# Kernel optimization log

Measured on AMD Instinct MI355X. Metric: run time of the kernel, lower is better.

The kernel has to match this reference:

```python
import jax, jax.numpy as jnp
import numpy as np

B, S, H = 8, 2048, 1024   # batch, seq, hidden_size
E = 4                     # num_experts (world_size=1 -> all local)
C = 1024                  # kv_cache_size (cache_decrement=0 -> uniform pyramid)
R = 4                     # LoRA rank
ALPHA = 1.0
TOP_K = 2
TEMP = 1.0
KEEP = C // 2             # pyramid compressor keeps top-half by importance


def _lora(z, A, Bm):
    # LoRALayer: (z @ A) @ B scaled by alpha/rank
    return (z @ A) @ Bm * (ALPHA / A.shape[-1])


def setup_inputs() -> dict:
    key = jax.random.key(0)
    ks = jax.random.split(key, 24)
    w = lambda k, shp: jax.random.normal(k, shp, jnp.float32) * 0.02
    return {
        'x': jax.random.normal(ks[0], (B, S, H), jnp.float32),
        'query': jax.random.normal(ks[1], (B, S, H), jnp.float32),
        'Wg': w(ks[2], (H, E)), 'bg': jnp.zeros((E,), jnp.float32),
        'Wq': w(ks[3], (H, H)), 'bq': jnp.zeros((H,), jnp.float32),
        'Wk': w(ks[4], (H, H)), 'bk': jnp.zeros((H,), jnp.float32),
        'Aq': w(ks[5], (H, R)), 'Bq': w(ks[6], (R, H)),
        'Ak': w(ks[7], (H, R)), 'Bk': w(ks[8], (R, H)),
        'We': w(ks[9], (E, H, H)), 'be': jnp.zeros((E, H), jnp.float32),
        'Ae': w(ks[10], (E, H, R)), 'Be': w(ks[11], (E, R, H)),
        'Av': w(ks[12], (E, H, R)), 'Bv': w(ks[13], (E, R, H)),
        'cache_keys': jax.random.normal(ks[14], (E, C, H), jnp.float32),
        'cache_values': jax.random.normal(ks[15], (E, C, H), jnp.float32),
        'cache_imp': jax.random.uniform(ks[16], (E, C), jnp.float32),
    }


def reference(x, query, Wg, bg, Wq, bq, Wk, bk, Aq, Bq, Ak, Bk,
              We, be, Ae, Be, Av, Bv, cache_keys, cache_values, cache_imp):
    # ---- AdaptiveRouter: softmax gate, top-2 renormalized, load-balance loss ----
    probs = jax.nn.softmax((x @ Wg + bg) / TEMP, axis=-1)             # [B,S,E]
    tw, ti = jax.lax.top_k(probs, TOP_K)                              # [B,S,K]
    twn = tw / tw.sum(-1, keepdims=True)
    onehot = jax.nn.one_hot(ti, E, dtype=x.dtype)                     # [B,S,K,E]
    routing = jnp.einsum('bsk,bske->bse', twn, onehot)                # [B,S,E]
    lb_loss = E * jnp.sum(probs.mean((0, 1)) * onehot.mean((0, 1, 2)))

    # ---- compute_token_importance (query provided): LoRA-augmented q/k attention ----
    q = query @ Wq + bq + _lora(query, Aq, Bq)
    k = x @ Wk + bk + _lora(x, Ak, Bk)
    att = jax.nn.softmax(jnp.einsum('bqh,bkh->bqk', q, k) / np.sqrt(H).astype(np.float32), axis=-1)
    importance = att.sum(axis=1)                                      # [B,S] column sums

    # ---- per-expert LoRA forward + pyramid-compressed cache read ----
    def expert_fn(We_i, be_i, Ae_i, Be_i, Av_i, Bv_i, cv_i, ci_i):
        eo = x @ We_i + be_i + _lora(x, Ae_i, Be_i)                   # [B,S,H]
        idx = jax.lax.top_k(ci_i, KEEP)[1]                            # keep top-half by importance
        vals = cv_i[idx]                                              # [KEEP,H] irregular gather
        vals = vals + _lora(vals, Av_i, Bv_i)                         # value LoRA on compressed cache
        return eo + jax.lax.stop_gradient(vals.mean(0))               # cached values are detached

    outs = jax.vmap(expert_fn)(We, be, Ae, Be, Av, Bv, cache_values, cache_imp)  # [E,B,S,H]
    expert_output = jnp.einsum('ebsh,bse->bsh', outs, routing)

    # ---- cache update at ptr=0 (detached buffer mutation -> returned new state) ----
    sg = jax.lax.stop_gradient
    new_keys = cache_keys.at[:, 0].set(jnp.broadcast_to(sg(x.mean((0, 1))), (E, H)))
    new_values = cache_values.at[:, 0].set(sg(outs.mean((1, 2))))
    new_imp = cache_imp.at[:, 0].set(sg(importance.mean()))
    return expert_output, lb_loss, new_keys, new_values, new_imp
```

## Files before the change

kernel.cpp:

```cpp
#include <hip/hip_runtime.h>

constexpr int kH    = 1024;
constexpr int kNT   = 16384;
constexpr int kE    = 4;
constexpr int kC    = 1024;
constexpr int kR    = 4;
constexpr int kKeep = 512;
constexpr float kLoraScale = 0.25f;
constexpr int kCapTiles = 136;
constexpr int kCapRows  = kCapTiles * 128;
constexpr int kNB      = kNT / 256;

constexpr size_t WS_RW     = 0;
constexpr size_t WS_G      = 65536;
constexpr size_t WS_XSUM   = 393216;
constexpr size_t WS_SHADOW = 394240;
constexpr size_t WS_TU     = 394752;
constexpr size_t WS_VBAR   = 394784;
constexpr size_t WS_FX     = 398880;
constexpr size_t WS_NEWV0  = 402976;
constexpr size_t WS_MSK    = 407072;
constexpr size_t WS_GBASE  = 411168;
constexpr size_t WS_BHIST  = 411176;
constexpr size_t WS_BOFF   = 411560;
constexpr size_t WS_RTPID  = 411944;
constexpr size_t WS_TPID   = 412088;
constexpr size_t WS_GRO    = 428472;
constexpr size_t WS_PERM   = 444856;
constexpr size_t WS_WCAT   = 462264;
constexpr size_t WS_AEXT   = 482744;
constexpr size_t WS_AEXTG  = 744888;
constexpr size_t WS_BEXT   = 1023416;
constexpr size_t WS_WET    = 1039800;
constexpr size_t WS_XG     = 3136952;

constexpr size_t OUT_LB = 16777216;
constexpr size_t OUT_NK = 16777217;

typedef __attribute__((ext_vector_type(8))) short bf16x8;
typedef __attribute__((ext_vector_type(4))) float f32x4;

__device__ __forceinline__ float wred(float v) {
#pragma unroll
  for (int off = 32; off; off >>= 1) v += __shfl_xor(v, off);
  return v;
}

__device__ __forceinline__ ushort f2bf(float f) {
  unsigned int u = __float_as_uint(f);
  u += 0x7FFFu + ((u >> 16) & 1u);
  return (ushort)(u >> 16);
}

__device__ __forceinline__ void gload16(const ushort* g, ushort* l) {
  __builtin_amdgcn_global_load_lds(
      (const __attribute__((address_space(1))) unsigned int*)g,
      (__attribute__((address_space(3))) unsigned int*)l, 16, 0, 0);
}

__device__ __forceinline__ int pid_a(int pid) { return pid < 3 ? 0 : (pid < 5 ? 1 : 2); }
__device__ __forceinline__ int pid_b(int pid) { return pid < 3 ? pid + 1 : (pid < 5 ? pid - 1 : 3); }

__global__ __launch_bounds__(256) void prep_k(
    const float* __restrict__ Wg, const float* __restrict__ Ae,
    const float* __restrict__ ci, const float* __restrict__ x,
    float* __restrict__ wcat, float* __restrict__ msk,
    float* __restrict__ xsum, int* __restrict__ perm) {
  __shared__ float imp[kC];
  const int b = blockIdx.x, tid = threadIdx.x;
  if (b < 80) {
    const int idx = b * 256 + tid;
    const int c = idx >> 10, k = idx & 1023;
    float v;
    if (c < 4) v = Wg[(size_t)k * 4 + c];
    else {
      const int e = (c - 4) >> 2, r = (c - 4) & 3;
      v = Ae[((size_t)e * kH + k) * kR + r];
    }
    wcat[(size_t)c * kH + k] = v;
  } else if (b < 96) {
    const int e = (b - 80) >> 2, part = (b - 80) & 3;
    const int c = part * 256 + tid;
    for (int i = tid; i < kC; i += 256) imp[i] = ci[(size_t)e * kC + i];
    __syncthreads();
    const float v = imp[c];
    int rank = 0;
    for (int c2 = 0; c2 < kC; ++c2) {
      const float v2 = imp[c2];
      rank += (v2 > v) || (v2 == v && c2 < c);
    }
    msk[(size_t)e * kC + c] = (rank < kKeep) ? 1.0f : 0.0f;
  } else if (b < 352) {
    const int rg = b - 96;
    const float* xp = x + (size_t)rg * 64 * kH + tid * 4;
    float s0 = 0.f, s1 = 0.f, s2 = 0.f, s3 = 0.f;
    for (int r = 0; r < 64; ++r) {
      const float4 v = *(const float4*)(xp + (size_t)r * kH);
      s0 += v.x; s1 += v.y; s2 += v.z; s3 += v.w;
    }
    atomicAdd(&xsum[tid * 4 + 0], s0);
    atomicAdd(&xsum[tid * 4 + 1], s1);
    atomicAdd(&xsum[tid * 4 + 2], s2);
    atomicAdd(&xsum[tid * 4 + 3], s3);
  } else {
    const int i = (b - 352) * 256 + tid;
    perm[i] = -1;
  }
}

__global__ __launch_bounds__(256) void router_gemm_k(
    const float* __restrict__ x, const float* __restrict__ wcat,
    float* __restrict__ G) {
  __shared__ float xs_l[128][64];
  __shared__ float wt_l[20][64];
  const int tid = threadIdx.x;
  const int t0 = blockIdx.x * 128;
  const int tok = tid & 127, half = tid >> 7, cb = half * 10;
  float acc[10] = {};
  for (int kc = 0; kc < 16; ++kc) {
#pragma unroll
    for (int i = 0; i < 8; ++i) {
      const int idx = tid + i * 256;
      const int stok = idx >> 4, sslot = idx & 15;
      const float4 v =
          *(const float4*)(x + (size_t)(t0 + stok) * kH + kc * 64 + sslot * 4);
      *(float4*)&xs_l[stok][((sslot + stok) & 15) * 4] = v;
    }
    for (int idx = tid; idx < 320; idx += 256) {
      const int c = idx >> 4, slot = idx & 15;
      *(float4*)&wt_l[c][slot * 4] =
          *(const float4*)(wcat + (size_t)c * kH + kc * 64 + slot * 4);
    }
    __syncthreads();
#pragma unroll
    for (int k4 = 0; k4 < 16; ++k4) {
      const float4 xv = *(const float4*)&xs_l[tok][((k4 + tok) & 15) * 4];
#pragma unroll
      for (int j = 0; j < 10; ++j) {
        const float4 wv = *(const float4*)&wt_l[cb + j][k4 * 4];
        acc[j] += xv.x * wv.x + xv.y * wv.y + xv.z * wv.z + xv.w * wv.w;
      }
    }
    __syncthreads();
  }
#pragma unroll
  for (int j = 0; j < 10; ++j)
    G[(size_t)(cb + j) * kNT + t0 + tok] = acc[j];
}

__global__ __launch_bounds__(256) void router_fin_k(
    const float* __restrict__ G, const float* __restrict__ bg,
    float* __restrict__ rw, float* __restrict__ shadow,
    int* __restrict__ tpid, int* __restrict__ bhist,
    ushort* __restrict__ aext) {
  __shared__ float swacc[8];
  __shared__ int ihist[6];
  const int tid = threadIdx.x;
  const int t = blockIdx.x * 256 + tid;
  const int lane = tid & 63;
  if (tid < 8) swacc[tid] = 0.f;
  if (tid < 6) ihist[tid] = 0;
  __syncthreads();
  float lg[kE];
#pragma unroll
  for (int e = 0; e < kE; ++e) lg[e] = G[(size_t)e * kNT + t] + bg[e];
  float la[kE][kR];
#pragma unroll
  for (int e = 0; e < kE; ++e)
#pragma unroll
    for (int r = 0; r < kR; ++r)
      la[e][r] = G[(size_t)(4 + e * 4 + r) * kNT + t];
  const float mx = fmaxf(fmaxf(lg[0], lg[1]), fmaxf(lg[2], lg[3]));
  float ex[kE], se = 0.f;
#pragma unroll
  for (int e = 0; e < kE; ++e) { ex[e] = __expf(lg[e] - mx); se += ex[e]; }
  float pr[kE];
#pragma unroll
  for (int e = 0; e < kE; ++e) pr[e] = ex[e] / se;
  int e1 = 0;
#pragma unroll
  for (int e = 1; e < kE; ++e) if (pr[e] > pr[e1]) e1 = e;
  int e2 = (e1 == 0) ? 1 : 0;
#pragma unroll
  for (int e = 0; e < kE; ++e) if (e != e1 && pr[e] > pr[e2]) e2 = e;
  const float s2 = pr[e1] + pr[e2];
  float rwv[kE] = {0.f, 0.f, 0.f, 0.f};
  rwv[e1] = pr[e1] / s2; rwv[e2] = pr[e2] / s2;
  *(float4*)(rw + (size_t)t * kE) = make_float4(rwv[0], rwv[1], rwv[2], rwv[3]);
  const int lo = min(e1, e2), hi = max(e1, e2);
  const int pid = (lo == 0) ? hi - 1 : ((lo == 1) ? hi + 1 : 5);
  tpid[t] = pid;
  __align__(16) ushort o[32];
#pragma unroll
  for (int e = 0; e < kE; ++e) o[e] = f2bf(rwv[e]);
#pragma unroll
  for (int e = 0; e < kE; ++e)
#pragma unroll
    for (int r = 0; r < kR; ++r)
      o[4 + e * 4 + r] = f2bf(kLoraScale * rwv[e] * la[e][r]);
#pragma unroll
  for (int i = 20; i < 32; ++i) o[i] = 0;
#pragma unroll
  for (int q = 0; q < 4; ++q)
    *(float4*)&aext[(size_t)t * 32 + q * 8] = *(float4*)&o[q * 8];
  float vals[8];
#pragma unroll
  for (int e = 0; e < kE; ++e) {
    vals[e] = pr[e];
    vals[4 + e] = ((e == e1) ? 1.f : 0.f) + ((e == e2) ? 1.f : 0.f);
  }
#pragma unroll
  for (int j = 0; j < 8; ++j) {
    vals[j] = wred(vals[j]);
    if (lane == 0) atomicAdd(&swacc[j], vals[j]);
  }
  atomicAdd(&ihist[pid], 1);
  __syncthreads();
  if (tid < 8) atomicAdd(&shadow[(blockIdx.x & 63) * 8 + tid], swacc[tid]);
  if (tid < 6) bhist[blockIdx.x * 6 + tid] = ihist[tid];
}

__global__ __launch_bounds__(256) void pscan_k(const int* __restrict__ bhist,
                                               int* __restrict__ gbase,
                                               int* __restrict__ boff,
                                               int* __restrict__ rtpid) {
  __shared__ int pcnt_s[6];
  const int tid = threadIdx.x;
  if (tid < 6) {
    int run = 0;
    for (int b = 0; b < kNB; ++b) {
      boff[b * 6 + tid] = run;
      run += bhist[b * 6 + tid];
    }
    pcnt_s[tid] = run;
  }
  __syncthreads();
  if (tid == 0) {
    int base = 0;
    for (int g = 0; g < 6; ++g) {
      gbase[g] = base;
      const int tiles = (pcnt_s[g] + 127) >> 7;
      for (int ti = 0; ti < tiles; ++ti) rtpid[(base >> 7) + ti] = g;
      base += tiles << 7;
    }
    for (int i = base >> 7; i < kCapTiles; ++i) rtpid[i] = -1;
  }
  __syncthreads();
  if (tid < 6) {
    const int gb = gbase[tid];
    for (int b = 0; b < kNB; ++b) boff[b * 6 + tid] += gb;
  }
}

__global__ __launch_bounds__(256) void slot_k(const int* __restrict__ tpid,
                                              const int* __restrict__ boff,
                                              int* __restrict__ gro,
                                              int* __restrict__ perm) {
  __shared__ int wcnt[4][6];
  const int tid = threadIdx.x, w = tid >> 6, lane = tid & 63;
  const int t = blockIdx.x * 256 + tid;
  const int pid = tpid[t];
  unsigned long long mymask = 0;
  int cnt[6];
#pragma unroll
  for (int g = 0; g < 6; ++g) {
    const unsigned long long m = __ballot(pid == g);
    cnt[g] = __popcll(m);
    if (g == pid) mymask = m;
  }
  if (lane < 6) wcnt[w][lane] = cnt[lane];
  const int rank_in_wave =
      __popcll(mymask & ((lane == 63) ? 0x7FFFFFFFFFFFFFFFULL
                                      : ((1ULL << lane) - 1ULL)));
  __syncthreads();
  int base = 0;
  for (int w2 = 0; w2 < w; ++w2) base += wcnt[w2][pid];
  const int grow = boff[blockIdx.x * 6 + pid] + base + rank_in_wave;
  gro[t] = grow;
  perm[grow] = t;
}

__global__ __launch_bounds__(256) void aux3_k(
    const float* __restrict__ x, const float* __restrict__ rw,
    const int* __restrict__ tpid, const ushort* __restrict__ aext,
    const int* __restrict__ gro, ushort* __restrict__ xg,
    ushort* __restrict__ aextg, const float* __restrict__ We,
    const float* __restrict__ xsum, ushort* __restrict__ wet,
    float* __restrict__ fx, const float* __restrict__ cv,
    const float* __restrict__ msk, float* __restrict__ vbar) {
  __shared__ ushort tile[64][72];
  __shared__ float fxl[16][64];
  __shared__ float xml[64];
  const int b = blockIdx.x, tid = threadIdx.x;
  if (b < 4096) {
    const int wave = tid >> 6, lane = tid & 63;
    const int t = b * 4 + wave;
    const int pid = tpid[t];
    const int grow = gro[t];
    const float wa = rw[(size_t)t * 4 + pid_a(pid)];
    const float wb = rw[(size_t)t * 4 + pid_b(pid)];
#pragma unroll
    for (int q = 0; q < 4; ++q) {
      const int c = q * 256 + lane * 4;
      const float4 v = *(const float4*)(x + (size_t)t * kH + c);
      ushort4 ua, ub;
      ua.x = f2bf(wa * v.x); ua.y = f2bf(wa * v.y);
      ua.z = f2bf(wa * v.z); ua.w = f2bf(wa * v.w);
      ub.x = f2bf(wb * v.x); ub.y = f2bf(wb * v.y);
      ub.z = f2bf(wb * v.z); ub.w = f2bf(wb * v.w);
      *(ushort4*)(xg + (size_t)grow * 2048 + c) = ua;
      *(ushort4*)(xg + (size_t)grow * 2048 + 1024 + c) = ub;
    }
    if (lane < 4)
      *(float4*)&aextg[(size_t)grow * 32 + lane * 8] =
          *(const float4*)&aext[(size_t)t * 32 + lane * 8];
  } else if (b < 5120) {
    const int bp = b - 4096;
    const int jb = bp & 15, kb = (bp >> 4) & 15, e = bp >> 8;
    const int rr = tid >> 4, cq = tid & 15;
    if (tid < 64) xml[tid] = xsum[kb * 64 + tid] * (1.0f / kNT);
    __syncthreads();
    float fxp[4] = {};
#pragma unroll
    for (int p = 0; p < 4; ++p) {
      const int k = kb * 64 + p * 16 + rr;
      const float4 v = *(const float4*)&We[((size_t)e * kH + k) * kH + jb * 64 + cq * 4];
      tile[p * 16 + rr][cq * 4 + 0] = f2bf(v.x);
      tile[p * 16 + rr][cq * 4 + 1] = f2bf(v.y);
      tile[p * 16 + rr][cq * 4 + 2] = f2bf(v.z);
      tile[p * 16 + rr][cq * 4 + 3] = f2bf(v.w);
      const float xm = xml[p * 16 + rr];
      fxp[0] += xm * v.x; fxp[1] += xm * v.y; fxp[2] += xm * v.z; fxp[3] += xm * v.w;
    }
    *(float4*)&fxl[rr][cq * 4] = make_float4(fxp[0], fxp[1], fxp[2], fxp[3]);
    __syncthreads();
    if (tid < 64) {
      float s = 0.f;
#pragma unroll
      for (int r2 = 0; r2 < 16; ++r2) s += fxl[r2][tid];
      atomicAdd(&fx[(size_t)e * kH + jb * 64 + tid], s);
    }
#pragma unroll
    for (int p = 0; p < 4; ++p) {
      const int j = jb * 64 + p * 16 + rr;
      ushort4 u;
      u.x = tile[cq * 4 + 0][p * 16 + rr];
      u.y = tile[cq * 4 + 1][p * 16 + rr];
      u.z = tile[cq * 4 + 2][p * 16 + rr];
      u.w = tile[cq * 4 + 3][p * 16 + rr];
      *(ushort4*)&wet[((size_t)e * kH + j) * kH + kb * 64 + cq * 4] = u;
    }
  } else {
    const int bp = b - 5120;
    const int e = bp & 3, rc = bp >> 2;
    const float* base = cv + (size_t)e * kC * kH + (size_t)rc * 32 * kH + tid * 4;
    const float* m = msk + (size_t)e * kC + rc * 32;
    float s0 = 0.f, s1 = 0.f, s2 = 0.f, s3 = 0.f;
#pragma unroll 8
    for (int r = 0; r < 32; ++r) {
      const float mr = m[r];
      const float4 v = *(const float4*)(base + (size_t)r * kH);
      s0 += mr * v.x; s1 += mr * v.y; s2 += mr * v.z; s3 += mr * v.w;
    }
    const float sc = 1.0f / kKeep;
    atomicAdd(&vbar[(size_t)e * kH + tid * 4 + 0], s0 * sc);
    atomicAdd(&vbar[(size_t)e * kH + tid * 4 + 1], s1 * sc);
    atomicAdd(&vbar[(size_t)e * kH + tid * 4 + 2], s2 * sc);
    atomicAdd(&vbar[(size_t)e * kH + tid * 4 + 3], s3 * sc);
  }
}

__global__ __launch_bounds__(256) void tufin_k(
    const float* __restrict__ vbar, const float* __restrict__ xsum,
    const float* __restrict__ Av, const float* __restrict__ Ae,
    const float* __restrict__ be, const float* __restrict__ Bv,
    const float* __restrict__ Bee, const float* __restrict__ fx,
    float* __restrict__ newv0_ws, ushort* __restrict__ bext) {
  __shared__ float red[256];
  __shared__ float tus[8];
  const int e = blockIdx.x, tid = threadIdx.x;
  float p[8] = {};
#pragma unroll
  for (int q = 0; q < 4; ++q) {
    const int h = tid * 4 + q;
    const float vb = vbar[(size_t)e * kH + h];
    const float xm = xsum[h] * (1.0f / kNT);
    const float4 av = *(const float4*)(Av + ((size_t)e * kH + h) * kR);
    const float4 ae = *(const float4*)(Ae + ((size_t)e * kH + h) * kR);
    p[0] += vb * av.x; p[1] += vb * av.y; p[2] += vb * av.z; p[3] += vb * av.w;
    p[4] += xm * ae.x; p[5] += xm * ae.y; p[6] += xm * ae.z; p[7] += xm * ae.w;
  }
#pragma unroll
  for (int j = 0; j < 8; ++j) {
    red[tid] = p[j]; __syncthreads();
    for (int s2 = 128; s2; s2 >>= 1) {
      if (tid < s2) red[tid] += red[tid + s2];
      __syncthreads();
    }
    if (tid == 0) tus[j] = red[0];
    __syncthreads();
  }
  float t_[4], u_[4];
#pragma unroll
  for (int r = 0; r < kR; ++r) { t_[r] = tus[r]; u_[r] = tus[4 + r]; }
#pragma unroll
  for (int q = 0; q < 4; ++q) {
    const int col = q * 256 + tid;
    float lv = 0.f, le = 0.f;
#pragma unroll
    for (int r = 0; r < kR; ++r) {
      lv += t_[r] * Bv[((size_t)e * kR + r) * kH + col];
      le += u_[r] * Bee[((size_t)e * kR + r) * kH + col];
    }
    const float mv = vbar[(size_t)e * kH + col] + kLoraScale * lv;
    const float bias = be[(size_t)e * kH + col] + mv;
    newv0_ws[(size_t)e * kH + col] = fx[(size_t)e * kH + col] + kLoraScale * le + bias;
    bext[(size_t)col * 32 + e] = f2bf(bias);
#pragma unroll
    for (int r = 0; r < kR; ++r)
      bext[(size_t)col * 32 + 4 + e * 4 + r] =
          f2bf(Bee[((size_t)e * kR + r) * kH + col]);
    if (e == 0)
#pragma unroll
      for (int i = 20; i < 32; ++i) bext[(size_t)col * 32 + i] = 0;
  }
}

__global__ __launch_bounds__(256, 2) void moe_gemm_pair_k(
    const ushort* __restrict__ xg, const ushort* __restrict__ wet,
    const ushort* __restrict__ aextg, const ushort* __restrict__ bext,
    const int* __restrict__ rtpid, const int* __restrict__ perm,
    float* __restrict__ out) {
  const int bid = blockIdx.x;
  const int gid = (bid & 7) * 136 + (bid >> 3);
  const int rt = gid >> 3, ct = gid & 7;
  const int pid = rtpid[rt];
  if (pid < 0) return;
  __shared__ __align__(16) ushort As[2][128 * 32];
  __shared__ __align__(16) ushort Bs[2][128 * 32];
  __shared__ int perm_s[128];
  const int tid = threadIdx.x;
  const int lane = tid & 63, wave = tid >> 6;
  const int wm = wave >> 1, wn = wave & 1;
  const int r0 = rt * 128, c0 = ct * 128;
  const int ea = pid_a(pid), eb = pid_b(pid);
  if (tid < 128) perm_s[tid] = perm[r0 + tid];

  const int srow = lane >> 2;
  const int sslot = lane & 3;

  auto stage = [&](int buf, int kt) {
#pragma unroll
    for (int i = 0; i < 2; ++i) {
      const int j0 = wave * 32 + i * 16;
      const int r = j0 + srow;
      const int slot = sslot ^ ((r >> 1) & 3);
      const ushort* srcA;
      const ushort* srcB;
      if (kt < 64) {
        const int e = (kt < 32) ? ea : eb;
        const int ko = ((kt & 31) * 32) + ((kt < 32) ? 0 : 1024);
        srcA = xg + (size_t)(r0 + r) * 2048 + ko + slot * 8;
        srcB = wet + ((size_t)e * kH + c0 + r) * kH + (kt & 31) * 32 + slot * 8;
      } else {
        srcA = aextg + (size_t)(r0 + r) * 32 + slot * 8;
        srcB = bext + (size_t)(c0 + r) * 32 + slot * 8;
      }
      gload16(srcA, &As[buf][j0 * 32]);
      gload16(srcB, &Bs[buf][j0 * 32]);
    }
  };

  f32x4 acc[4][4] = {};
  stage(0, 0);
  asm volatile("s_waitcnt vmcnt(0)" ::: "memory");
  __syncthreads();

  const int rA = lane & 15;
  const int fslot = lane >> 4;
  int buf = 0;
  for (int kt = 0; kt <= 64; ++kt) {
    if (kt < 64) stage(buf ^ 1, kt + 1);
    bf16x8 a[4], b[4];
#pragma unroll
    for (int m = 0; m < 4; ++m) {
      const int r = wm * 64 + m * 16 + rA;
      const int sl = fslot ^ ((r >> 1) & 3);
      a[m] = *(const bf16x8*)&As[buf][r * 32 + sl * 8];
    }
#pragma unroll
    for (int n = 0; n < 4; ++n) {
      const int r = wn * 64 + n * 16 + rA;
      const int sl = fslot ^ ((r >> 1) & 3);
      b[n] = *(const bf16x8*)&Bs[buf][r * 32 + sl * 8];
    }
#pragma unroll
    for (int m = 0; m < 4; ++m)
#pragma unroll
      for (int n = 0; n < 4; ++n)
        acc[m][n] = __builtin_amdgcn_mfma_f32_16x16x32_bf16(a[m], b[n], acc[m][n], 0, 0, 0);
    if (kt < 64) asm volatile("s_waitcnt vmcnt(0)" ::: "memory");
    __syncthreads();
    buf ^= 1;
  }

#pragma unroll
  for (int m = 0; m < 4; ++m) {
#pragma unroll
    for (int v = 0; v < 4; ++v) {
      const int rl = wm * 64 + m * 16 + (lane >> 4) * 4 + v;
      const int tok = perm_s[rl];
      if (tok >= 0) {
        float* orow = out + (size_t)tok * kH + c0 + wn * 64 + (lane & 15);
#pragma unroll
        for (int n = 0; n < 4; ++n) orow[n * 16] = acc[m][n][v];
      }
    }
  }
}

__global__ __launch_bounds__(256) void copyfix_k(
    const float* __restrict__ ck, const float* __restrict__ cv,
    const float* __restrict__ ci, const float* __restrict__ xsum,
    const float* __restrict__ newv0, const float* __restrict__ shadow,
    float* __restrict__ out) {
  const size_t NK = (size_t)kE * kC * kH;
  const size_t idx = (size_t)blockIdx.x * 256 + threadIdx.x;
  if (idx < NK) {
    const size_t c = (idx >> 10) & (kC - 1), h = idx & (kH - 1);
    out[OUT_NK + idx] = (c == 0) ? xsum[h] * (1.0f / kNT) : ck[idx];
  } else if (idx < 2 * NK) {
    const size_t j = idx - NK;
    const size_t e = j >> 20, c = (j >> 10) & (kC - 1), h = j & (kH - 1);
    out[OUT_NK + idx] = (c == 0) ? newv0[e * kH + h] : cv[j];
  } else if (idx < 2 * NK + (size_t)kE * kC) {
    const size_t j = idx - 2 * NK;
    out[OUT_NK + idx] = ((j & (kC - 1)) == 0) ? 1.0f : ci[j];
  } else if (idx == 2 * NK + (size_t)kE * kC) {
    float lb = 0.f;
#pragma unroll
    for (int e = 0; e < kE; ++e) {
      float ps = 0.f, cn = 0.f;
      for (int s2 = 0; s2 < 64; ++s2) {
        ps += shadow[s2 * 8 + e];
        cn += shadow[s2 * 8 + 4 + e];
      }
      lb += (ps * (1.0f / kNT)) * (cn * (1.0f / (kNT * 2.0f)));
    }
    out[OUT_LB] = kE * lb;
  }
}

extern "C" void kernel_launch(void* const* d_in, const int* in_sizes, int n_in,
                              void* d_out, int out_size, void* d_ws, size_t ws_size,
                              hipStream_t stream) {
  const float* x   = (const float*)d_in[0];
  const float* Wg  = (const float*)d_in[2];
  const float* bg  = (const float*)d_in[3];
  const float* We  = (const float*)d_in[12];
  const float* be  = (const float*)d_in[13];
  const float* Ae  = (const float*)d_in[14];
  const float* Bee = (const float*)d_in[15];
  const float* Av  = (const float*)d_in[16];
  const float* Bv  = (const float*)d_in[17];
  const float* ck  = (const float*)d_in[18];
  const float* cv  = (const float*)d_in[19];
  const float* ci  = (const float*)d_in[20];
  float* ws  = (float*)d_ws;
  float* out = (float*)d_out;

  int* tpid  = (int*)(ws + WS_TPID);
  int* bhist = (int*)(ws + WS_BHIST);
  int* boff  = (int*)(ws + WS_BOFF);
  int* gbase = (int*)(ws + WS_GBASE);
  int* rtpid = (int*)(ws + WS_RTPID);
  int* gro   = (int*)(ws + WS_GRO);
  int* perm  = (int*)(ws + WS_PERM);
  ushort* aext  = (ushort*)(ws + WS_AEXT);
  ushort* aextg = (ushort*)(ws + WS_AEXTG);
  ushort* bext  = (ushort*)(ws + WS_BEXT);
  ushort* wet   = (ushort*)(ws + WS_WET);
  ushort* xg    = (ushort*)(ws + WS_XG);

  hipMemsetAsync(ws + WS_XSUM, 0, 9760 * sizeof(float), stream);
  prep_k<<<420, 256, 0, stream>>>(Wg, Ae, ci, x, ws + WS_WCAT, ws + WS_MSK,
                                  ws + WS_XSUM, perm);
  router_gemm_k<<<kNT / 128, 256, 0, stream>>>(x, ws + WS_WCAT, ws + WS_G);
  router_fin_k<<<kNB, 256, 0, stream>>>(ws + WS_G, bg, ws + WS_RW,
                                        ws + WS_SHADOW, tpid, bhist, aext);
  pscan_k<<<1, 256, 0, stream>>>(bhist, gbase, boff, rtpid);
  slot_k<<<kNB, 256, 0, stream>>>(tpid, boff, gro, perm);
  aux3_k<<<5248, 256, 0, stream>>>(x, ws + WS_RW, tpid, aext, gro, xg, aextg,
                                   We, ws + WS_XSUM, wet, ws + WS_FX, cv,
                                   ws + WS_MSK, ws + WS_VBAR);
  tufin_k<<<kE, 256, 0, stream>>>(ws + WS_VBAR, ws + WS_XSUM, Av, Ae, be, Bv,
                                  Bee, ws + WS_FX, ws + WS_NEWV0, bext);
  moe_gemm_pair_k<<<kCapTiles * 8, 256, 0, stream>>>(
      xg, wet, aextg, bext, rtpid, perm, out);
  copyfix_k<<<32785, 256, 0, stream>>>(ck, cv, ci, ws + WS_XSUM, ws + WS_NEWV0,
                                       ws + WS_SHADOW, out);
}
```

Measured before the change: 332.0 us.

## Regroup kernels to overlap router GEMM, weight transpose and cache copy

Result: slower. 379.5 us (+14.3%).

```diff
diff --git a/kernel.cpp b/kernel.cpp
--- a/kernel.cpp
+++ b/kernel.cpp
@@ -108,44 +108,105 @@
   }
 }
 
-__global__ __launch_bounds__(256) void router_gemm_k(
+__global__ __launch_bounds__(256) void rgwv_k(
     const float* __restrict__ x, const float* __restrict__ wcat,
-    float* __restrict__ G) {
-  __shared__ float xs_l[128][64];
-  __shared__ float wt_l[20][64];
-  const int tid = threadIdx.x;
-  const int t0 = blockIdx.x * 128;
-  const int tok = tid & 127, half = tid >> 7, cb = half * 10;
-  float acc[10] = {};
-  for (int kc = 0; kc < 16; ++kc) {
-#pragma unroll
-    for (int i = 0; i < 8; ++i) {
-      const int idx = tid + i * 256;
-      const int stok = idx >> 4, sslot = idx & 15;
-      const float4 v =
-          *(const float4*)(x + (size_t)(t0 + stok) * kH + kc * 64 + sslot * 4);
-      *(float4*)&xs_l[stok][((sslot + stok) & 15) * 4] = v;
-    }
-    for (int idx = tid; idx < 320; idx += 256) {
-      const int c = idx >> 4, slot = idx & 15;
-      *(float4*)&wt_l[c][slot * 4] =
-          *(const float4*)(wcat + (size_t)c * kH + kc * 64 + slot * 4);
-    }
+    float* __restrict__ G, const float* __restrict__ We,
+    const float* __restrict__ xsum, ushort* __restrict__ wet,
+    float* __restrict__ fx, const float* __restrict__ cv,
+    const float* __restrict__ msk, float* __restrict__ vbar) {
+  union Smem {
+    struct { float xs[128][64]; float wt[20][64]; } rg;
+    struct { ushort tile[64][72]; float fxl[16][64]; float xml[64]; } wf;
+  };
+  __shared__ Smem sm;
+  const int b = blockIdx.x, tid = threadIdx.x;
+  if (b < 128) {
+    const int t0 = b * 128;
+    const int tok = tid & 127, half = tid >> 7, cb = half * 10;
+    float acc[10] = {};
+    for (int kc = 0; kc < 16; ++kc) {
+#pragma unroll
+      for (int i = 0; i < 8; ++i) {
+        const int idx = tid + i * 256;
+        const int stok = idx >> 4, sslot = idx & 15;
+        const float4 v =
+            *(const float4*)(x + (size_t)(t0 + stok) * kH + kc * 64 + sslot * 4);
+        *(float4*)&sm.rg.xs[stok][((sslot + stok) & 15) * 4] = v;
+      }
+      for (int idx = tid; idx < 320; idx += 256) {
+        const int c = idx >> 4, slot = idx & 15;
+        *(float4*)&sm.rg.wt[c][slot * 4] =
+            *(const float4*)(wcat + (size_t)c * kH + kc * 64 + slot * 4);
+      }
+      __syncthreads();
+#pragma unroll
+      for (int k4 = 0; k4 < 16; ++k4) {
+        const float4 xv = *(const float4*)&sm.rg.xs[tok][((k4 + tok) & 15) * 4];
+#pragma unroll
+        for (int j = 0; j < 10; ++j) {
+          const float4 wv = *(const float4*)&sm.rg.wt[cb + j][k4 * 4];
+          acc[j] += xv.x * wv.x + xv.y * wv.y + xv.z * wv.z + xv.w * wv.w;
+        }
+      }
+      __syncthreads();
+    }
+#pragma unroll
+    for (int j = 0; j < 10; ++j)
+      G[(size_t)(cb + j) * kNT + t0 + tok] = acc[j];
+  } else if (b < 1152) {
+    const int bp = b - 128;
+    const int jb = bp & 15, kb = (bp >> 4) & 15, e = bp >> 8;
+    const int rr = tid >> 4, cq = tid & 15;
+    if (tid < 64) sm.wf.xml[tid] = xsum[kb * 64 + tid] * (1.0f / kNT);
     __syncthreads();
-#pragma unroll
-    for (int k4 = 0; k4 < 16; ++k4) {
-      const float4 xv = *(const float4*)&xs_l[tok][((k4 + tok) & 15) * 4];
-#pragma unroll
-      for (int j = 0; j < 10; ++j) {
-        const float4 wv = *(const float4*)&wt_l[cb + j][k4 * 4];
-        acc[j] += xv.x * wv.x + xv.y * wv.y + xv.z * wv.z + xv.w * wv.w;
-      }
-    }
+    float fxp[4] = {};
+#pragma unroll
+    for (int p = 0; p < 4; ++p) {
+      const int k = kb * 64 + p * 16 + rr;
+      const float4 v = *(const float4*)&We[((size_t)e * kH + k) * kH + jb * 64 + cq * 4];
+      sm.wf.tile[p * 16 + rr][cq * 4 + 0] = f2bf(v.x);
+      sm.wf.tile[p * 16 + rr][cq * 4 + 1] = f2bf(v.y);
+      sm.wf.tile[p * 16 + rr][cq * 4 + 2] = f2bf(v.z);
+      sm.wf.tile[p * 16 + rr][cq * 4 + 3] = f2bf(v.w);
+      const float xm = sm.wf.xml[p * 16 + rr];
+      fxp[0] += xm * v.x; fxp[1] += xm * v.y; fxp[2] += xm * v.z; fxp[3] += xm * v.w;
+    }
+    *(float4*)&sm.wf.fxl[rr][cq * 4] = make_float4(fxp[0], fxp[1], fxp[2], fxp[3]);
     __syncthreads();
-  }
-#pragma unroll
-  for (int j = 0; j < 10; ++j)
-    G[(size_t)(cb + j) * kNT + t0 + tok] = acc[j];
+    if (tid < 64) {
+      float s = 0.f;
+#pragma unroll
+      for (int r2 = 0; r2 < 16; ++r2) s += sm.wf.fxl[r2][tid];
+      atomicAdd(&fx[(size_t)e * kH + jb * 64 + tid], s);
+    }
+#pragma unroll
+    for (int p = 0; p < 4; ++p) {
+      const int j = jb * 64 + p * 16 + rr;
+      ushort4 u;
+      u.x = sm.wf.tile[cq * 4 + 0][p * 16 + rr];
+      u.y = sm.wf.tile[cq * 4 + 1][p * 16 + rr];
+      u.z = sm.wf.tile[cq * 4 + 2][p * 16 + rr];
+      u.w = sm.wf.tile[cq * 4 + 3][p * 16 + rr];
+      *(ushort4*)&wet[((size_t)e * kH + j) * kH + kb * 64 + cq * 4] = u;
+    }
+  } else {
+    const int bp = b - 1152;
+    const int e = bp & 3, rc = bp >> 2;
+    const float* base = cv + (size_t)e * kC * kH + (size_t)rc * 32 * kH + tid * 4;
+    const float* m = msk + (size_t)e * kC + rc * 32;
+    float s0 = 0.f, s1 = 0.f, s2 = 0.f, s3 = 0.f;
+#pragma unroll 8
+    for (int r = 0; r < 32; ++r) {
+      const float mr = m[r];
+      const float4 v = *(const float4*)(base + (size_t)r * kH);
+      s0 += mr * v.x; s1 += mr * v.y; s2 += mr * v.z; s3 += mr * v.w;
+    }
+    const float sc = 1.0f / kKeep;
+    atomicAdd(&vbar[(size_t)e * kH + tid * 4 + 0], s0 * sc);
+    atomicAdd(&vbar[(size_t)e * kH + tid * 4 + 1], s1 * sc);
+    atomicAdd(&vbar[(size_t)e * kH + tid * 4 + 2], s2 * sc);
+    atomicAdd(&vbar[(size_t)e * kH + tid * 4 + 3], s3 * sc);
+  }
 }
 
 __global__ __launch_bounds__(256) void router_fin_k(
@@ -252,194 +313,164 @@
   }
 }
 
-__global__ __launch_bounds__(256) void slot_k(const int* __restrict__ tpid,
-                                              const int* __restrict__ boff,
-                                              int* __restrict__ gro,
-                                              int* __restrict__ perm) {
-  __shared__ int wcnt[4][6];
-  const int tid = threadIdx.x, w = tid >> 6, lane = tid & 63;
-  const int t = blockIdx.x * 256 + tid;
-  const int pid = tpid[t];
-  unsigned long long mymask = 0;
-  int cnt[6];
-#pragma unroll
-  for (int g = 0; g < 6; ++g) {
-    const unsigned long long m = __ballot(pid == g);
-    cnt[g] = __popcll(m);
-    if (g == pid) mymask = m;
-  }
-  if (lane < 6) wcnt[w][lane] = cnt[lane];
-  const int rank_in_wave =
-      __popcll(mymask & ((lane == 63) ? 0x7FFFFFFFFFFFFFFFULL
-                                      : ((1ULL << lane) - 1ULL)));
-  __syncthreads();
-  int base = 0;
-  for (int w2 = 0; w2 < w; ++w2) base += wcnt[w2][pid];
-  const int grow = boff[blockIdx.x * 6 + pid] + base + rank_in_wave;
-  gro[t] = grow;
-  perm[grow] = t;
-}
-
-__global__ __launch_bounds__(256) void aux3_k(
-    const float* __restrict__ x, const float* __restrict__ rw,
-    const int* __restrict__ tpid, const ushort* __restrict__ aext,
-    const int* __restrict__ gro, ushort* __restrict__ xg,
-    ushort* __restrict__ aextg, const float* __restrict__ We,
-    const float* __restrict__ xsum, ushort* __restrict__ wet,
-    float* __restrict__ fx, const float* __restrict__ cv,
-    const float* __restrict__ msk, float* __restrict__ vbar) {
-  __shared__ ushort tile[64][72];
-  __shared__ float fxl[16][64];
-  __shared__ float xml[64];
-  const int b = blockIdx.x, tid = threadIdx.x;
-  if (b < 4096) {
-    const int wave = tid >> 6, lane = tid & 63;
-    const int t = b * 4 + wave;
-    const int pid = tpid[t];
-    const int grow = gro[t];
-    const float wa = rw[(size_t)t * 4 + pid_a(pid)];
-    const float wb = rw[(size_t)t * 4 + pid_b(pid)];
-#pragma unroll
-    for (int q = 0; q < 4; ++q) {
-      const int c = q * 256 + lane * 4;
-      const float4 v = *(const float4*)(x + (size_t)t * kH + c);
-      ushort4 ua, ub;
-      ua.x = f2bf(wa * v.x); ua.y = f2bf(wa * v.y);
-      ua.z = f2bf(wa * v.z); ua.w = f2bf(wa * v.w);
-      ub.x = f2bf(wb * v.x); ub.y = f2bf(wb * v.y);
-      ub.z = f2bf(wb * v.z); ub.w = f2bf(wb * v.w);
-      *(ushort4*)(xg + (size_t)grow * 2048 + c) = ua;
-      *(ushort4*)(xg + (size_t)grow * 2048 + 1024 + c) = ub;
-    }
-    if (lane < 4)
-      *(float4*)&aextg[(size_t)grow * 32 + lane * 8] =
-          *(const float4*)&aext[(size_t)t * 32 + lane * 8];
-  } else if (b < 5120) {
-    const int bp = b - 4096;
-    const int jb = bp & 15, kb = (bp >> 4) & 15, e = bp >> 8;
-    const int rr = tid >> 4, cq = tid & 15;
-    if (tid < 64) xml[tid] = xsum[kb * 64 + tid] * (1.0f / kNT);
-    __syncthreads();
-    float fxp[4] = {};
-#pragma unroll
-    for (int p = 0; p < 4; ++p) {
-      const int k = kb * 64 + p * 16 + rr;
-      const float4 v = *(const float4*)&We[((size_t)e * kH + k) * kH + jb * 64 + cq * 4];
-      tile[p * 16 + rr][cq * 4 + 0] = f2bf(v.x);
-      tile[p * 16 + rr][cq * 4 + 1] = f2bf(v.y);
-      tile[p * 16 + rr][cq * 4 + 2] = f2bf(v.z);
-      tile[p * 16 + rr][cq * 4 + 3] = f2bf(v.w);
-      const float xm = xml[p * 16 + rr];
-      fxp[0] += xm * v.x; fxp[1] += xm * v.y; fxp[2] += xm * v.z; fxp[3] += xm * v.w;
-    }
-    *(float4*)&fxl[rr][cq * 4] = make_float4(fxp[0], fxp[1], fxp[2], fxp[3]);
-    __syncthreads();
-    if (tid < 64) {
-      float s = 0.f;
-#pragma unroll
-      for (int r2 = 0; r2 < 16; ++r2) s += fxl[r2][tid];
-      atomicAdd(&fx[(size_t)e * kH + jb * 64 + tid], s);
-    }
-#pragma unroll
-    for (int p = 0; p < 4; ++p) {
-      const int j = jb * 64 + p * 16 + rr;
-      ushort4 u;
-      u.x = tile[cq * 4 + 0][p * 16 + rr];
-      u.y = tile[cq * 4 + 1][p * 16 + rr];
-      u.z = tile[cq * 4 + 2][p * 16 + rr];
-      u.w = tile[cq * 4 + 3][p * 16 + rr];
-      *(ushort4*)&wet[((size_t)e * kH + j) * kH + kb * 64 + cq * 4] = u;
-    }
-  } else {
-    const int bp = b - 5120;
-    const int e = bp & 3, rc = bp >> 2;
-    const float* base = cv + (size_t)e * kC * kH + (size_t)rc * 32 * kH + tid * 4;
-    const float* m = msk + (size_t)e * kC + rc * 32;
-    float s0 = 0.f, s1 = 0.f, s2 = 0.f, s3 = 0.f;
-#pragma unroll 8
-    for (int r = 0; r < 32; ++r) {
-      const float mr = m[r];
-      const float4 v = *(const float4*)(base + (size_t)r * kH);
-      s0 += mr * v.x; s1 += mr * v.y; s2 += mr * v.z; s3 += mr * v.w;
-    }
-    const float sc = 1.0f / kKeep;
-    atomicAdd(&vbar[(size_t)e * kH + tid * 4 + 0], s0 * sc);
-    atomicAdd(&vbar[(size_t)e * kH + tid * 4 + 1], s1 * sc);
-    atomicAdd(&vbar[(size_t)e * kH + tid * 4 + 2], s2 * sc);
-    atomicAdd(&vbar[(size_t)e * kH + tid * 4 + 3], s3 * sc);
-  }
-}
-
-__global__ __launch_bounds__(256) void tufin_k(
+__global__ __launch_bounds__(256) void slot_tufin_k(
+    const int* __restrict__ tpid, const int* __restrict__ boff,
+    int* __restrict__ gro, int* __restrict__ perm,
     const float* __restrict__ vbar, const float* __restrict__ xsum,
     const float* __restrict__ Av, const float* __restrict__ Ae,
     const float* __restrict__ be, const float* __restrict__ Bv,
     const float* __restrict__ Bee, const float* __restrict__ fx,
     float* __restrict__ newv0_ws, ushort* __restrict__ bext) {
+  __shared__ int wcnt[4][6];
   __shared__ float red[256];
   __shared__ float tus[8];
-  const int e = blockIdx.x, tid = threadIdx.x;
-  float p[8] = {};
+  const int b = blockIdx.x, tid = threadIdx.x;
+  if (b < 64) {
+    const int w = tid >> 6, lane = tid & 63;
+    const int t = b * 256 + tid;
+    const int pid = tpid[t];
+    unsigned long long mymask = 0;
+    int cnt[6];
+#pragma unroll
+    for (int g = 0; g < 6; ++g) {
+      const unsigned long long m = __ballot(pid == g);
+      cnt[g] = __popcll(m);
+      if (g == pid) mymask = m;
+    }
+    if (lane < 6) wcnt[w][lane] = cnt[lane];
+    const int rank_in_wave =
+        __popcll(mymask & ((lane == 63) ? 0x7FFFFFFFFFFFFFFFULL
+                                        : ((1ULL << lane) - 1ULL)));
+    __syncthreads();
+    int base = 0;
+    for (int w2 = 0; w2 < w; ++w2) base += wcnt[w2][pid];
+    const int grow = boff[b * 6 + pid] + base + rank_in_wave;
+    gro[t] = grow;
+    perm[grow] = t;
+  } else {
+    const int e = b - 64;
+    float p[8] = {};
+#pragma unroll
+    for (int q = 0; q < 4; ++q) {
+      const int h = tid * 4 + q;
+      const float vb = vbar[(size_t)e * kH + h];
+      const float xm = xsum[h] * (1.0f / kNT);
+      const float4 av = *(const float4*)(Av + ((size_t)e * kH + h) * kR);
+      const float4 ae = *(const float4*)(Ae + ((size_t)e * kH + h) * kR);
+      p[0] += vb * av.x; p[1] += vb * av.y; p[2] += vb * av.z; p[3] += vb * av.w;
+      p[4] += xm * ae.x; p[5] += xm * ae.y; p[6] += xm * ae.z; p[7] += xm * ae.w;
+    }
+#pragma unroll
+    for (int j = 0; j < 8; ++j) {
+      red[tid] = p[j]; __syncthreads();
+      for (int s2 = 128; s2; s2 >>= 1) {
+        if (tid < s2) red[tid] += red[tid + s2];
+        __syncthreads();
+      }
+      if (tid == 0) tus[j] = red[0];
+      __syncthreads();
+    }
+    float t_[4], u_[4];
+#pragma unroll
+    for (int r = 0; r < kR; ++r) { t_[r] = tus[r]; u_[r] = tus[4 + r]; }
+#pragma unroll
+    for (int q = 0; q < 4; ++q) {
+      const int col = q * 256 + tid;
+      float lv = 0.f, le = 0.f;
+#pragma unroll
+      for (int r = 0; r < kR; ++r) {
+        lv += t_[r] * Bv[((size_t)e * kR + r) * kH + col];
+        le += u_[r] * Bee[((size_t)e * kR + r) * kH + col];
+      }
+      const float mv = vbar[(size_t)e * kH + col] + kLoraScale * lv;
+      const float bias = be[(size_t)e * kH + col] + mv;
+      newv0_ws[(size_t)e * kH + col] =
+          fx[(size_t)e * kH + col] + kLoraScale * le + bias;
+      bext[(size_t)col * 32 + e] = f2bf(bias);
+#pragma unroll
+      for (int r = 0; r < kR; ++r)
+        bext[(size_t)col * 32 + 4 + e * 4 + r] =
+            f2bf(Bee[((size_t)e * kR + r) * kH + col]);
+      if (e == 0)
+#pragma unroll
+        for (int i = 20; i < 32; ++i) bext[(size_t)col * 32 + i] = 0;
+    }
+  }
+}
+
+__global__ __launch_bounds__(256) void xg_k(
+    const float* __restrict__ x, const float* __restrict__ rw,
+    const int* __restrict__ tpid, const ushort* __restrict__ aext,
+    const int* __restrict__ gro, ushort* __restrict__ xg,
+    ushort* __restrict__ aextg) {
+  const int wave = threadIdx.x >> 6, lane = threadIdx.x & 63;
+  const int t = blockIdx.x * 4 + wave;
+  const int pid = tpid[t];
+  const int grow = gro[t];
+  const float wa = rw[(size_t)t * 4 + pid_a(pid)];
+  const float wb = rw[(size_t)t * 4 + pid_b(pid)];
 #pragma unroll
   for (int q = 0; q < 4; ++q) {
-    const int h = tid * 4 + q;
-    const float vb = vbar[(size_t)e * kH + h];
-    const float xm = xsum[h] * (1.0f / kNT);
-    const float4 av = *(const float4*)(Av + ((size_t)e * kH + h) * kR);
-    const float4 ae = *(const float4*)(Ae + ((size_t)e * kH + h) * kR);
-    p[0] += vb * av.x; p[1] += vb * av.y; p[2] += vb * av.z; p[3] += vb * av.w;
-    p[4] += xm * ae.x; p[5] += xm * ae.y; p[6] += xm * ae.z; p[7] += xm * ae.w;
-  }
-#pragma unroll
-  for (int j = 0; j < 8; ++j) {
-    red[tid] = p[j]; __syncthreads();
-    for (int s2 = 128; s2; s2 >>= 1) {
-      if (tid < s2) red[tid] += red[tid + s2];
-      __syncthreads();
-    }
-    if (tid == 0) tus[j] = red[0];
-    __syncthreads();
-  }
-  float t_[4], u_[4];
-#pragma unroll
-  for (int r = 0; r < kR; ++r) { t_[r] = tus[r]; u_[r] = tus[4 + r]; }
-#pragma unroll
-  for (int q = 0; q < 4; ++q) {
-    const int col = q * 256 + tid;
-    float lv = 0.f, le = 0.f;
-#pragma unroll
-    for (int r = 0; r < kR; ++r) {
-      lv += t_[r] * Bv[((size_t)e * kR + r) * kH + col];
-      le += u_[r] * Bee[((size_t)e * kR + r) * kH + col];
-    }
-    const float mv = vbar[(size_t)e * kH + col] + kLoraScale * lv;
-    const float bias = be[(size_t)e * kH + col] + mv;
-    newv0_ws[(size_t)e * kH + col] = fx[(size_t)e * kH + col] + kLoraScale * le + bias;
-    bext[(size_t)col * 32 + e] = f2bf(bias);
-#pragma unroll
-    for (int r = 0; r < kR; ++r)
-      bext[(size_t)col * 32 + 4 + e * 4 + r] =
-          f2bf(Bee[((size_t)e * kR + r) * kH + col]);
-    if (e == 0)
-#pragma unroll
-      for (int i = 20; i < 32; ++i) bext[(size_t)col * 32 + i] = 0;
-  }
-}
-
-__global__ __launch_bounds__(256, 2) void moe_gemm_pair_k(
+    const int c = q * 256 + lane * 4;
+    const float4 v = *(const float4*)(x + (size_t)t * kH + c);
+    ushort4 ua, ub;
+    ua.x = f2bf(wa * v.x); ua.y = f2bf(wa * v.y);
+    ua.z = f2bf(wa * v.z); ua.w = f2bf(wa * v.w);
+    ub.x = f2bf(wb * v.x); ub.y = f2bf(wb * v.y);
+    ub.z = f2bf(wb * v.z); ub.w = f2bf(wb * v.w);
+    *(ushort4*)(xg + (size_t)grow * 2048 + c) = ua;
+    *(ushort4*)(xg + (size_t)grow * 2048 + 1024 + c) = ub;
+  }
+  if (lane < 4)
+    *(float4*)&aextg[(size_t)grow * 32 + lane * 8] =
+        *(const float4*)&aext[(size_t)t * 32 + lane * 8];
+}
+
+__global__ __launch_bounds__(256, 2) void gemm_copyfix_k(
     const ushort* __restrict__ xg, const ushort* __restrict__ wet,
     const ushort* __restrict__ aextg, const ushort* __restrict__ bext,
     const int* __restrict__ rtpid, const int* __restrict__ perm,
+    const float* __restrict__ ck, const float* __restrict__ cv,
+    const float* __restrict__ ci, const float* __restrict__ xsum,
+    const float* __restrict__ newv0, const float* __restrict__ shadow,
     float* __restrict__ out) {
+  __shared__ __align__(16) ushort As[2][128 * 32];
+  __shared__ __align__(16) ushort Bs[2][128 * 32];
+  __shared__ int perm_s[128];
+  const int tid = threadIdx.x;
+  if (blockIdx.x >= 1088) {
+    const size_t NK = (size_t)kE * kC * kH;
+    const size_t idx = (size_t)(blockIdx.x - 1088) * 256 + tid;
+    if (idx < NK) {
+      const size_t c = (idx >> 10) & (kC - 1), h = idx & (kH - 1);
+      out[OUT_NK + idx] = (c == 0) ? xsum[h] * (1.0f / kNT) : ck[idx];
+    } else if (idx < 2 * NK) {
+      const size_t j = idx - NK;
+      const size_t e = j >> 20, c = (j >> 10) & (kC - 1), h = j & (kH - 1);
+      out[OUT_NK + idx] = (c == 0) ? newv0[e * kH + h] : cv[j];
+    } else if (idx < 2 * NK + (size_t)kE * kC) {
+      const size_t j = idx - 2 * NK;
+      out[OUT_NK + idx] = ((j & (kC - 1)) == 0) ? 1.0f : ci[j];
+    } else if (idx == 2 * NK + (size_t)kE * kC) {
+      float lb = 0.f;
+#pragma unroll
+      for (int e = 0; e < kE; ++e) {
+        float ps = 0.f, cn = 0.f;
+        for (int s2 = 0; s2 < 64; ++s2) {
+          ps += shadow[s2 * 8 + e];
+          cn += shadow[s2 * 8 + 4 + e];
+        }
+        lb += (ps * (1.0f / kNT)) * (cn * (1.0f / (kNT * 2.0f)));
+      }
+      out[OUT_LB] = kE * lb;
+    }
+    return;
+  }
   const int bid = blockIdx.x;
   const int gid = (bid & 7) * 136 + (bid >> 3);
   const int rt = gid >> 3, ct = gid & 7;
   const int pid = rtpid[rt];
   if (pid < 0) return;
-  __shared__ __align__(16) ushort As[2][128 * 32];
-  __shared__ __align__(16) ushort Bs[2][128 * 32];
-  __shared__ int perm_s[128];
-  const int tid = threadIdx.x;
   const int lane = tid & 63, wave = tid >> 6;
   const int wm = wave >> 1, wn = wave & 1;
   const int r0 = rt * 128, c0 = ct * 128;
@@ -516,38 +547,6 @@
         for (int n = 0; n < 4; ++n) orow[n * 16] = acc[m][n][v];
       }
     }
-  }
-}
-
-__global__ __launch_bounds__(256) void copyfix_k(
-    const float* __restrict__ ck, const float* __restrict__ cv,
-    const float* __restrict__ ci, const float* __restrict__ xsum,
-    const float* __restrict__ newv0, const float* __restrict__ shadow,
-    float* __restrict__ out) {
-  const size_t NK = (size_t)kE * kC * kH;
-  const size_t idx = (size_t)blockIdx.x * 256 + threadIdx.x;
-  if (idx < NK) {
-    const size_t c = (idx >> 10) & (kC - 1), h = idx & (kH - 1);
-    out[OUT_NK + idx] = (c == 0) ? xsum[h] * (1.0f / kNT) : ck[idx];
-  } else if (idx < 2 * NK) {
-    const size_t j = idx - NK;
-    const size_t e = j >> 20, c = (j >> 10) & (kC - 1), h = j & (kH - 1);
-    out[OUT_NK + idx] = (c == 0) ? newv0[e * kH + h] : cv[j];
-  } else if (idx < 2 * NK + (size_t)kE * kC) {
-    const size_t j = idx - 2 * NK;
-    out[OUT_NK + idx] = ((j & (kC - 1)) == 0) ? 1.0f : ci[j];
-  } else if (idx == 2 * NK + (size_t)kE * kC) {
-    float lb = 0.f;
-#pragma unroll
-    for (int e = 0; e < kE; ++e) {
-      float ps = 0.f, cn = 0.f;
-      for (int s2 = 0; s2 < 64; ++s2) {
-        ps += shadow[s2 * 8 + e];
-        cn += shadow[s2 * 8 + 4 + e];
-      }
-      lb += (ps * (1.0f / kNT)) * (cn * (1.0f / (kNT * 2.0f)));
-    }
-    out[OUT_LB] = kE * lb;
   }
 }
 
@@ -585,18 +584,17 @@
   hipMemsetAsync(ws + WS_XSUM, 0, 9760 * sizeof(float), stream);
   prep_k<<<420, 256, 0, stream>>>(Wg, Ae, ci, x, ws + WS_WCAT, ws + WS_MSK,
                                   ws + WS_XSUM, perm);
-  router_gemm_k<<<kNT / 128, 256, 0, stream>>>(x, ws + WS_WCAT, ws + WS_G);
+  rgwv_k<<<1280, 256, 0, stream>>>(x, ws + WS_WCAT, ws + WS_G, We,
+                                   ws + WS_XSUM, wet, ws + WS_FX, cv,
+                                   ws + WS_MSK, ws + WS_VBAR);
   router_fin_k<<<kNB, 256, 0, stream>>>(ws + WS_G, bg, ws + WS_RW,
                                         ws + WS_SHADOW, tpid, bhist, aext);
   pscan_k<<<1, 256, 0, stream>>>(bhist, gbase, boff, rtpid);
-  slot_k<<<kNB, 256, 0, stream>>>(tpid, boff, gro, perm);
-  aux3_k<<<5248, 256, 0, stream>>>(x, ws + WS_RW, tpid, aext, gro, xg, aextg,
-                                   We, ws + WS_XSUM, wet, ws + WS_FX, cv,
-                                   ws + WS_MSK, ws + WS_VBAR);
-  tufin_k<<<kE, 256, 0, stream>>>(ws + WS_VBAR, ws + WS_XSUM, Av, Ae, be, Bv,
-                                  Bee, ws + WS_FX, ws + WS_NEWV0, bext);
-  moe_gemm_pair_k<<<kCapTiles * 8, 256, 0, stream>>>(
-      xg, wet, aextg, bext, rtpid, perm, out);
-  copyfix_k<<<32785, 256, 0, stream>>>(ck, cv, ci, ws + WS_XSUM, ws + WS_NEWV0,
-                                       ws + WS_SHADOW, out);
-}
+  slot_tufin_k<<<68, 256, 0, stream>>>(tpid, boff, gro, perm, ws + WS_VBAR,
+                                       ws + WS_XSUM, Av, Ae, be, Bv, Bee,
+                                       ws + WS_FX, ws + WS_NEWV0, bext);
+  xg_k<<<kNT / 4, 256, 0, stream>>>(x, ws + WS_RW, tpid, aext, gro, xg, aextg);
+  gemm_copyfix_k<<<1088 + 32785, 256, 0, stream>>>(
+      xg, wet, aextg, bext, rtpid, perm, ck, cv, ci, ws + WS_XSUM,
+      ws + WS_NEWV0, ws + WS_SHADOW, out);
+}
```
